# Kernel tuning notes

Measured on AMD Instinct MI355X. Metric: run time of the kernel, lower is better.

## Reference

```python
import jax, jax.numpy as jnp
import numpy as np

B, N, HID = 8, 512, 512
HEADS, HD = 16, 32
FFN, DEMB = 2048, 64
EPS = 1e-5


def layer_norm(x, g, b):
    mu = jnp.mean(x, axis=-1, keepdims=True)
    var = jnp.var(x, axis=-1, keepdims=True)
    return (x - mu) * jax.lax.rsqrt(var + EPS) * g + b


def setup_inputs() -> dict:
    key = jax.random.key(0)
    ks = jax.random.split(key, 16)
    s = lambda fan_in: 1.0 / np.sqrt(fan_in)
    return {
        "x": jax.random.normal(ks[0], (B, N, HID), jnp.float32),
        "distance_features": jax.random.normal(ks[1], (B, N, N, DEMB), jnp.float32),
        "edge_mask": jax.random.randint(ks[2], (B, N, N), 0, 2) > 0,
        "qkv_w": jax.random.uniform(ks[3], (HID, 3 * HID), jnp.float32, -s(HID), s(HID)),
        "qkv_b": jnp.zeros((3 * HID,), jnp.float32),
        "out_w": jax.random.uniform(ks[4], (HID, HID), jnp.float32, -s(HID), s(HID)),
        "out_b": jnp.zeros((HID,), jnp.float32),
        "dist_w": jax.random.uniform(ks[5], (DEMB, HEADS), jnp.float32, -s(DEMB), s(DEMB)),
        "dist_b": jnp.zeros((HEADS,), jnp.float32),
        "ln1_g": jnp.ones((HID,), jnp.float32),
        "ln1_b": jnp.zeros((HID,), jnp.float32),
        "ln2_g": jnp.ones((HID,), jnp.float32),
        "ln2_b": jnp.zeros((HID,), jnp.float32),
        "ff1_w": jax.random.uniform(ks[6], (HID, FFN), jnp.float32, -s(HID), s(HID)),
        "ff1_b": jnp.zeros((FFN,), jnp.float32),
        "ff2_w": jax.random.uniform(ks[7], (FFN, HID), jnp.float32, -s(FFN), s(FFN)),
        "ff2_b": jnp.zeros((HID,), jnp.float32),
    }


def reference(x, distance_features, edge_mask, qkv_w, qkv_b, out_w, out_b,
              dist_w, dist_b, ln1_g, ln1_b, ln2_g, ln2_b,
              ff1_w, ff1_b, ff2_w, ff2_b):
    residual = x
    h = layer_norm(x, ln1_g, ln1_b)
    qkv = h @ qkv_w + qkv_b  # [B,N,3*HID]
    q, k, v = jnp.split(qkv, 3, axis=-1)
    q = q.reshape(B, N, HEADS, HD)
    k = k.reshape(B, N, HEADS, HD)
    v = v.reshape(B, N, HEADS, HD)
    scale = jnp.sqrt(jnp.float32(HD))
    scores = jnp.einsum('bihd,bjhd->bhij', q, k) / scale  # [B,H,N,N]
    bias = distance_features @ dist_w + dist_b  # [B,N,N,H]
    scores = scores + jnp.transpose(bias, (0, 3, 1, 2))
    neg = jnp.finfo(scores.dtype).min
    scores = jnp.where(edge_mask[:, None, :, :], scores, neg)
    attn = jax.nn.softmax(scores, axis=-1)
    ctx = jnp.einsum('bhij,bjhd->bihd', attn, v).reshape(B, N, HID)
    x = residual + ctx @ out_w + out_b
    y = layer_norm(x, ln2_g, ln2_b)
    ff = jax.nn.gelu(y @ ff1_w + ff1_b, approximate=False) @ ff2_w + ff2_b
    return x + ff
```

## Files before the change

### kernel.cpp

```cpp
#include <hip/hip_runtime.h>
#include <cstddef>
#include <cstdint>

#define B_     8
#define N_     512
#define HID_   512
#define HEADS_ 16
#define HD_    32
#define FFN_   2048
#define DEMB_  64
#define ROWS   (B_*N_)

typedef unsigned short u16;
typedef short bf16x8 __attribute__((ext_vector_type(8)));
typedef float f32x4  __attribute__((ext_vector_type(4)));
typedef short short8v __attribute__((ext_vector_type(8)));
typedef short short4v __attribute__((ext_vector_type(4)));

__device__ __forceinline__ u16 f2bf(float f) {
  unsigned u = __float_as_uint(f);
  u += 0x7fffu + ((u >> 16) & 1u);
  return (u16)(u >> 16);
}
__device__ __forceinline__ float bf2f(u16 b) {
  return __uint_as_float(((unsigned)b) << 16);
}

__device__ __forceinline__ void gload16(const void* g, void* l) {
  __builtin_amdgcn_global_load_lds(
      (const __attribute__((address_space(1))) unsigned int*)g,
      (__attribute__((address_space(3))) unsigned int*)l, 16, 0, 0);
}

__global__ void detect_mask_kernel(const unsigned char* __restrict__ m,
                                   int* __restrict__ flag) {
  int t = blockIdx.x * blockDim.x + threadIdx.x;
  if ((t & 3) != 0) {
    if (m[t] != 0) atomicOr(flag, 1);
  }
}

__global__ __launch_bounds__(256) void ln_kernel(const float* __restrict__ x,
                                                 const float* __restrict__ g,
                                                 const float* __restrict__ bt,
                                                 u16* __restrict__ y) {
  const int lane = threadIdx.x & 63;
  const int row  = blockIdx.x * 4 + (threadIdx.x >> 6);
  const float* xr = x + (size_t)row * HID_;
  float4 v0 = *(const float4*)(xr + lane * 8);
  float4 v1 = *(const float4*)(xr + lane * 8 + 4);
  float s = v0.x + v0.y + v0.z + v0.w + v1.x + v1.y + v1.z + v1.w;
  float q = v0.x*v0.x + v0.y*v0.y + v0.z*v0.z + v0.w*v0.w
          + v1.x*v1.x + v1.y*v1.y + v1.z*v1.z + v1.w*v1.w;
  #pragma unroll
  for (int off = 32; off > 0; off >>= 1) {
    s += __shfl_xor(s, off, 64);
    q += __shfl_xor(q, off, 64);
  }
  const float mean = s * (1.0f / HID_);
  const float var  = q * (1.0f / HID_) - mean * mean;
  const float rs   = rsqrtf(var + 1e-5f);
  const float4 g0 = *(const float4*)(g + lane * 8);
  const float4 g1 = *(const float4*)(g + lane * 8 + 4);
  const float4 b0 = *(const float4*)(bt + lane * 8);
  const float4 b1 = *(const float4*)(bt + lane * 8 + 4);
  short8v o;
  o[0] = (short)f2bf((v0.x - mean) * rs * g0.x + b0.x);
  o[1] = (short)f2bf((v0.y - mean) * rs * g0.y + b0.y);
  o[2] = (short)f2bf((v0.z - mean) * rs * g0.z + b0.z);
  o[3] = (short)f2bf((v0.w - mean) * rs * g0.w + b0.w);
  o[4] = (short)f2bf((v1.x - mean) * rs * g1.x + b1.x);
  o[5] = (short)f2bf((v1.y - mean) * rs * g1.y + b1.y);
  o[6] = (short)f2bf((v1.z - mean) * rs * g1.z + b1.z);
  o[7] = (short)f2bf((v1.w - mean) * rs * g1.w + b1.w);
  *(short8v*)(y + (size_t)row * HID_ + lane * 8) = o;
}

__global__ __launch_bounds__(256) void wt_kernel(const float* __restrict__ W,
                                                 u16* __restrict__ Wt,
                                                 int K, int N) {
  __shared__ float tile[32][33];
  const int t = threadIdx.x;
  const int n0 = blockIdx.x * 32, k0 = blockIdx.y * 32;
  const int tx = t & 31, ty = t >> 5;
  #pragma unroll
  for (int i = 0; i < 4; ++i)
    tile[ty + 8 * i][tx] = W[(size_t)(k0 + ty + 8 * i) * N + n0 + tx];
  __syncthreads();
  #pragma unroll
  for (int i = 0; i < 4; ++i) {
    const int n = ty + 8 * i;
    Wt[(size_t)(n0 + n) * K + k0 + tx] = f2bf(tile[tx][n]);
  }
}

template <int ACT, bool HAS_RES, bool OUT_BF16>
__global__ __launch_bounds__(256) void mfma_gemm(
    const u16* __restrict__ A, const u16* __restrict__ Wt,
    const float* __restrict__ bias, const float* __restrict__ res,
    void* __restrict__ Cout, int N, int K) {
  __shared__ __align__(16) u16 As[128 * 64];
  __shared__ __align__(16) u16 Bs[128 * 64];
  const int t    = threadIdx.x;
  const int wid  = t >> 6, lane = t & 63;
  const int wr   = wid >> 1, wc = wid & 1;
  const int m0   = blockIdx.y * 128, n0 = blockIdx.x * 128;
  const int srow8 = lane >> 3;
  const int sslot = (lane & 7) ^ srow8;

  f32x4 zero = {0.f, 0.f, 0.f, 0.f};
  f32x4 acc[4][4];
  #pragma unroll
  for (int m = 0; m < 4; ++m)
    #pragma unroll
    for (int n = 0; n < 4; ++n) acc[m][n] = zero;

  for (int kt = 0; kt < K; kt += 64) {
    __syncthreads();
    #pragma unroll
    for (int i = 0; i < 4; ++i) {
      const int rbase = wid * 32 + i * 8;
      const int r = rbase + srow8;
      gload16(A  + (size_t)(m0 + r) * K + kt + sslot * 8, &As[rbase * 64]);
      gload16(Wt + (size_t)(n0 + r) * K + kt + sslot * 8, &Bs[rbase * 64]);
    }
    __syncthreads();
    #pragma unroll
    for (int kk = 0; kk < 2; ++kk) {
      bf16x8 a[4], b[4];
      #pragma unroll
      for (int m = 0; m < 4; ++m) {
        const int row = wr * 64 + m * 16 + (lane & 15);
        const int s   = (kk * 4 + (lane >> 4)) ^ (row & 7);
        a[m] = *(const bf16x8*)&As[row * 64 + s * 8];
      }
      #pragma unroll
      for (int n = 0; n < 4; ++n) {
        const int row = wc * 64 + n * 16 + (lane & 15);
        const int s   = (kk * 4 + (lane >> 4)) ^ (row & 7);
        b[n] = *(const bf16x8*)&Bs[row * 64 + s * 8];
      }
      #pragma unroll
      for (int m = 0; m < 4; ++m)
        #pragma unroll
        for (int n = 0; n < 4; ++n)
          acc[m][n] = __builtin_amdgcn_mfma_f32_16x16x32_bf16(
              a[m], b[n], acc[m][n], 0, 0, 0);
    }
  }
  #pragma unroll
  for (int n = 0; n < 4; ++n) {
    const int col = n0 + wc * 64 + n * 16 + (lane & 15);
    const float bb = bias[col];
    #pragma unroll
    for (int m = 0; m < 4; ++m) {
      #pragma unroll
      for (int j = 0; j < 4; ++j) {
        const int row = m0 + wr * 64 + m * 16 + (lane >> 4) * 4 + j;
        float v = acc[m][n][j] + bb;
        if (ACT == 1) v = 0.5f * v * (1.0f + erff(v * 0.70710678118654752f));
        const size_t off = (size_t)row * N + col;
        if (HAS_RES) v += res[off];
        if (OUT_BF16) ((u16*)Cout)[off] = f2bf(v);
        else          ((float*)Cout)[off] = v;
      }
    }
  }
}

__global__ __launch_bounds__(256) void bias_kernel(
    const float* __restrict__ df, const unsigned char* __restrict__ mask8,
    const float* __restrict__ dw, const float* __restrict__ db,
    const int* __restrict__ flag, u16* __restrict__ biasb) {
  __shared__ float dfs[128][68];
  const int t    = threadIdx.x;
  const int tile = blockIdx.x & 3;
  const int i    = (blockIdx.x >> 2) & 511;
  const int b    = blockIdx.x >> 11;
  const int j0   = tile * 128;
  const int h    = t >> 4;
  const int jt   = t & 15;

  const float4* gsrc =
      (const float4*)(df + (((size_t)b * N_ + i) * N_ + j0) * DEMB_);
  #pragma unroll
  for (int s = 0; s < 8; ++s) {
    const int f   = s * 256 + t;
    const int row = f >> 4, d4 = f & 15;
    *(float4*)&dfs[row][d4 * 4] = gsrc[f];
  }

  float4 w[16];
  #pragma unroll
  for (int d4 = 0; d4 < 16; ++d4) {
    w[d4].x = dw[(d4 * 4 + 0) * HEADS_ + h];
    w[d4].y = dw[(d4 * 4 + 1) * HEADS_ + h];
    w[d4].z = dw[(d4 * 4 + 2) * HEADS_ + h];
    w[d4].w = dw[(d4 * 4 + 3) * HEADS_ + h];
  }
  const float bh = db[h];
  const int fb = *flag;
  const int* mask32 = (const int*)mask8;
  const size_t mbase = ((size_t)b * N_ + i) * N_ + j0;
  u16* obase = biasb + (((size_t)b * HEADS_ + h) * N_ + i) * N_ + j0;
  __syncthreads();

  for (int s = 0; s < 8; ++s) {
    const int jl = s * 16 + jt;
    float a0 = 0.f, a1 = 0.f, a2 = 0.f, a3 = 0.f;
    #pragma unroll
    for (int d4 = 0; d4 < 16; ++d4) {
      const float4 v = *(const float4*)&dfs[jl][d4 * 4];
      a0 += v.x * w[d4].x;
      a1 += v.y * w[d4].y;
      a2 += v.z * w[d4].z;
      a3 += v.w * w[d4].w;
    }
    const float acc = (a0 + a1) + (a2 + a3) + bh;
    const bool mv = fb ? (mask8[mbase + jl] != 0) : (mask32[mbase + jl] != 0);
    obase[jl] = f2bf(mv ? acc : -1e30f);
  }
}

__global__ __launch_bounds__(256) void attn_kernel(
    const float* __restrict__ qkv, const u16* __restrict__ biasb,
    u16* __restrict__ ctx) {
  __shared__ union {
    u16 k[N_ * HD_];
    struct {
      float po[3][64][33];
      float pm[3][64];
      float pl[3][64];
    } c;
  } sm;
  const int t    = threadIdx.x;
  const int bx   = blockIdx.x;
  const int b    = bx >> 7;
  const int h    = (bx >> 3) & 15;
  const int iblk = bx & 7;
  const int jq   = t >> 6;
  const int r    = t & 63;
  const int i    = iblk * 64 + r;
  const size_t qbase = (size_t)b * N_ * (3 * HID_);

  for (int idx = t; idx < N_ * 8; idx += 256) {
    const int j = idx >> 3, f = idx & 7;
    const float4 kv = *(const float4*)(qkv + qbase + (size_t)j * (3 * HID_) +
                                       HID_ + h * HD_ + f * 4);
    short4v ks;
    ks[0] = (short)f2bf(kv.x); ks[1] = (short)f2bf(kv.y);
    ks[2] = (short)f2bf(kv.z); ks[3] = (short)f2bf(kv.w);
    *(short4v*)&sm.k[j * HD_ + f * 4] = ks;
  }
  __syncthreads();

  float q[HD_];
  {
    const float* qp = qkv + qbase + (size_t)i * (3 * HID_) + h * HD_;
    #pragma unroll
    for (int f = 0; f < 8; ++f) {
      const float4 v = *(const float4*)(qp + f * 4);
      q[f*4+0] = v.x * 0.17677669529663687f;
      q[f*4+1] = v.y * 0.17677669529663687f;
      q[f*4+2] = v.z * 0.17677669529663687f;
      q[f*4+3] = v.w * 0.17677669529663687f;
    }
  }
  const u16* brow = biasb + (((size_t)b * HEADS_ + h) * N_ + i) * N_ + jq * 128;
  const float* vbase = qkv + qbase + 2 * HID_ + h * HD_;
  float m = -3.0e38f, l = 0.f;
  float o[HD_];
  #pragma unroll
  for (int d = 0; d < HD_; ++d) o[d] = 0.f;

  for (int j8 = 0; j8 < 128; j8 += 8) {
    const short8v bq = *(const short8v*)(brow + j8);
    #pragma unroll
    for (int e = 0; e < 8; ++e) {
      const int j = jq * 128 + j8 + e;
      const u16* kr = &sm.k[j * HD_];
      float s = 0.f;
      #pragma unroll
      for (int c = 0; c < 4; ++c) {
        const short8v kk = *(const short8v*)(kr + c * 8);
        #pragma unroll
        for (int d = 0; d < 8; ++d)
          s += q[c*8+d] * bf2f((u16)kk[d]);
      }
      s += bf2f((u16)bq[e]);
      if (s - m > 8.0f) {
        const float corr = __expf(m - s);
        l *= corr;
        #pragma unroll
        for (int d = 0; d < HD_; ++d) o[d] *= corr;
        m = s;
      }
      const float p = __expf(s - m);
      l += p;
      const float4* vr = (const float4*)(vbase + (size_t)j * (3 * HID_));
      #pragma unroll
      for (int c = 0; c < 8; ++c) {
        const float4 vv = vr[c];
        o[c*4+0] += p * vv.x; o[c*4+1] += p * vv.y;
        o[c*4+2] += p * vv.z; o[c*4+3] += p * vv.w;
      }
    }
  }

  __syncthreads();
  if (jq > 0) {
    sm.c.pm[jq-1][r] = m;
    sm.c.pl[jq-1][r] = l;
    #pragma unroll
    for (int d = 0; d < HD_; ++d) sm.c.po[jq-1][r][d] = o[d];
  }
  __syncthreads();
  if (jq == 0) {
    #pragma unroll
    for (int p2 = 0; p2 < 3; ++p2) {
      const float m2 = sm.c.pm[p2][r], l2 = sm.c.pl[p2][r];
      const float mn = fmaxf(m, m2);
      const float c1 = __expf(m - mn), c2 = __expf(m2 - mn);
      l = l * c1 + l2 * c2;
      #pragma unroll
      for (int d = 0; d < HD_; ++d)
        o[d] = o[d] * c1 + sm.c.po[p2][r][d] * c2;
      m = mn;
    }
    const float inv = 1.0f / l;
    u16* cp = ctx + (((size_t)b * N_ + i) * HEADS_ + h) * HD_;
    #pragma unroll
    for (int f = 0; f < 4; ++f) {
      short8v v;
      #pragma unroll
      for (int e = 0; e < 8; ++e) v[e] = (short)f2bf(o[f*8+e] * inv);
      *(short8v*)(cp + f * 8) = v;
    }
  }
}

extern "C" void kernel_launch(void* const* d_in, const int* in_sizes, int n_in,
                              void* d_out, int out_size, void* d_ws, size_t ws_size,
                              hipStream_t stream) {
  const float* x      = (const float*)d_in[0];
  const float* df     = (const float*)d_in[1];
  const unsigned char* mask = (const unsigned char*)d_in[2];
  const float* qkv_w  = (const float*)d_in[3];
  const float* qkv_b  = (const float*)d_in[4];
  const float* out_w  = (const float*)d_in[5];
  const float* out_b  = (const float*)d_in[6];
  const float* dist_w = (const float*)d_in[7];
  const float* dist_b = (const float*)d_in[8];
  const float* ln1_g  = (const float*)d_in[9];
  const float* ln1_b  = (const float*)d_in[10];
  const float* ln2_g  = (const float*)d_in[11];
  const float* ln2_b  = (const float*)d_in[12];
  const float* ff1_w  = (const float*)d_in[13];
  const float* ff1_b  = (const float*)d_in[14];
  const float* ff2_w  = (const float*)d_in[15];
  const float* ff2_b  = (const float*)d_in[16];
  float* out = (float*)d_out;

  char* p = (char*)d_ws;
  auto alloc = [&](size_t bytes) {
    char* r = p;
    p += (bytes + 255) & ~(size_t)255;
    return r;
  };
  float* qkv    = (float*)alloc((size_t)ROWS * 3 * HID_ * 4);
  u16*   biasb  = (u16*)alloc((size_t)B_ * HEADS_ * N_ * N_ * 2);
  float* xa     = (float*)alloc((size_t)ROWS * HID_ * 4);
  u16*   h16    = (u16*)alloc((size_t)ROWS * HID_ * 2);
  u16*   ctx16  = (u16*)alloc((size_t)ROWS * HID_ * 2);
  u16*   y16    = (u16*)alloc((size_t)ROWS * HID_ * 2);
  u16*   ff116  = (u16*)alloc((size_t)ROWS * FFN_ * 2);
  u16*   qkv_wt = (u16*)alloc((size_t)3 * HID_ * HID_ * 2);
  u16*   out_wt = (u16*)alloc((size_t)HID_ * HID_ * 2);
  u16*   ff1_wt = (u16*)alloc((size_t)FFN_ * HID_ * 2);
  u16*   ff2_wt = (u16*)alloc((size_t)HID_ * FFN_ * 2);
  int*   flag   = (int*)alloc(sizeof(int));

  hipMemsetAsync(flag, 0, sizeof(int), stream);
  detect_mask_kernel<<<256, 256, 0, stream>>>(mask, flag);

  wt_kernel<<<dim3(3 * HID_ / 32, HID_ / 32), 256, 0, stream>>>(qkv_w, qkv_wt, HID_, 3 * HID_);
  wt_kernel<<<dim3(HID_ / 32, HID_ / 32), 256, 0, stream>>>(out_w, out_wt, HID_, HID_);
  wt_kernel<<<dim3(FFN_ / 32, HID_ / 32), 256, 0, stream>>>(ff1_w, ff1_wt, HID_, FFN_);
  wt_kernel<<<dim3(HID_ / 32, FFN_ / 32), 256, 0, stream>>>(ff2_w, ff2_wt, FFN_, HID_);

  ln_kernel<<<ROWS / 4, 256, 0, stream>>>(x, ln1_g, ln1_b, h16);
  mfma_gemm<0, false, false><<<dim3(3 * HID_ / 128, ROWS / 128), 256, 0, stream>>>(
      h16, qkv_wt, qkv_b, nullptr, qkv, 3 * HID_, HID_);
  bias_kernel<<<B_ * N_ * 4, 256, 0, stream>>>(df, mask, dist_w, dist_b, flag, biasb);
  attn_kernel<<<B_ * HEADS_ * 8, 256, 0, stream>>>(qkv, biasb, ctx16);
  mfma_gemm<0, true, false><<<dim3(HID_ / 128, ROWS / 128), 256, 0, stream>>>(
      ctx16, out_wt, out_b, x, xa, HID_, HID_);
  ln_kernel<<<ROWS / 4, 256, 0, stream>>>(xa, ln2_g, ln2_b, y16);
  mfma_gemm<1, false, true><<<dim3(FFN_ / 128, ROWS / 128), 256, 0, stream>>>(
      y16, ff1_wt, ff1_b, nullptr, ff116, FFN_, HID_);
  mfma_gemm<0, true, false><<<dim3(HID_ / 128, ROWS / 128), 256, 0, stream>>>(
      ff116, ff2_wt, ff2_b, xa, out, HID_, FFN_);
}
```

Before: 529.8 us.

## Merge weight-prep launches and stage bias outputs in LDS for vector stores

Measured after the change: 465.2 us. 1.14x faster.

```diff
diff --git a/kernel.cpp b/kernel.cpp
--- a/kernel.cpp
+++ b/kernel.cpp
@@ -32,11 +32,42 @@
       (__attribute__((address_space(3))) unsigned int*)l, 16, 0, 0);
 }
 
-__global__ void detect_mask_kernel(const unsigned char* __restrict__ m,
-                                   int* __restrict__ flag) {
-  int t = blockIdx.x * blockDim.x + threadIdx.x;
-  if ((t & 3) != 0) {
-    if (m[t] != 0) atomicOr(flag, 1);
+__device__ __forceinline__ void wt_tile(const float* __restrict__ W,
+                                        u16* __restrict__ Wt,
+                                        int K, int N, int tt, int tid) {
+  __shared__ float tile[32][33];
+  const int nt = N / 32;
+  const int n0 = (tt % nt) * 32, k0 = (tt / nt) * 32;
+  const int tx = tid & 31, ty = tid >> 5;
+  #pragma unroll
+  for (int i = 0; i < 4; ++i)
+    tile[ty + 8 * i][tx] = W[(size_t)(k0 + ty + 8 * i) * N + n0 + tx];
+  __syncthreads();
+  #pragma unroll
+  for (int i = 0; i < 4; ++i) {
+    const int n = ty + 8 * i;
+    Wt[(size_t)(n0 + n) * K + k0 + tx] = f2bf(tile[tx][n]);
+  }
+}
+
+__global__ __launch_bounds__(256) void prep_kernel(
+    const float* __restrict__ qkv_w, const float* __restrict__ out_w,
+    const float* __restrict__ ff1_w, const float* __restrict__ ff2_w,
+    u16* __restrict__ qkv_wt, u16* __restrict__ out_wt,
+    u16* __restrict__ ff1_wt, u16* __restrict__ ff2_wt,
+    const unsigned char* __restrict__ mask, int* __restrict__ flag) {
+  const int bid = blockIdx.x, t = threadIdx.x;
+  if (bid < 768) {
+    wt_tile(qkv_w, qkv_wt, HID_, 3 * HID_, bid, t);
+  } else if (bid < 1024) {
+    wt_tile(out_w, out_wt, HID_, HID_, bid - 768, t);
+  } else if (bid < 2048) {
+    wt_tile(ff1_w, ff1_wt, HID_, FFN_, bid - 1024, t);
+  } else if (bid < 3072) {
+    wt_tile(ff2_w, ff2_wt, FFN_, HID_, bid - 2048, t);
+  } else {
+    const int idx = (bid - 3072) * 256 + t;
+    if ((idx & 3) != 0 && mask[idx] != 0) atomicOr(flag, 1);
   }
 }
 
@@ -76,24 +107,6 @@
   *(short8v*)(y + (size_t)row * HID_ + lane * 8) = o;
 }
 
-__global__ __launch_bounds__(256) void wt_kernel(const float* __restrict__ W,
-                                                 u16* __restrict__ Wt,
-                                                 int K, int N) {
-  __shared__ float tile[32][33];
-  const int t = threadIdx.x;
-  const int n0 = blockIdx.x * 32, k0 = blockIdx.y * 32;
-  const int tx = t & 31, ty = t >> 5;
-  #pragma unroll
-  for (int i = 0; i < 4; ++i)
-    tile[ty + 8 * i][tx] = W[(size_t)(k0 + ty + 8 * i) * N + n0 + tx];
-  __syncthreads();
-  #pragma unroll
-  for (int i = 0; i < 4; ++i) {
-    const int n = ty + 8 * i;
-    Wt[(size_t)(n0 + n) * K + k0 + tx] = f2bf(tile[tx][n]);
-  }
-}
-
 template <int ACT, bool HAS_RES, bool OUT_BF16>
 __global__ __launch_bounds__(256) void mfma_gemm(
     const u16* __restrict__ A, const u16* __restrict__ Wt,
@@ -173,6 +186,8 @@
     const float* __restrict__ dw, const float* __restrict__ db,
     const int* __restrict__ flag, u16* __restrict__ biasb) {
   __shared__ float dfs[128][68];
+  __shared__ u16 obuf[HEADS_][128];
+  __shared__ unsigned char mbuf[128];
   const int t    = threadIdx.x;
   const int tile = blockIdx.x & 3;
   const int i    = (blockIdx.x >> 2) & 511;
@@ -186,8 +201,12 @@
   #pragma unroll
   for (int s = 0; s < 8; ++s) {
     const int f   = s * 256 + t;
-    const int row = f >> 4, d4 = f & 15;
-    *(float4*)&dfs[row][d4 * 4] = gsrc[f];
+    *(float4*)&dfs[f >> 4][(f & 15) * 4] = gsrc[f];
+  }
+  const int fb = *flag;
+  if (t < 128) {
+    const size_t midx = ((size_t)b * N_ + i) * N_ + j0 + t;
+    mbuf[t] = fb ? (mask8[midx] != 0) : (((const int*)mask8)[midx] != 0);
   }
 
   float4 w[16];
@@ -199,12 +218,9 @@
     w[d4].w = dw[(d4 * 4 + 3) * HEADS_ + h];
   }
   const float bh = db[h];
-  const int fb = *flag;
-  const int* mask32 = (const int*)mask8;
-  const size_t mbase = ((size_t)b * N_ + i) * N_ + j0;
-  u16* obase = biasb + (((size_t)b * HEADS_ + h) * N_ + i) * N_ + j0;
-  __syncthreads();
-
+  __syncthreads();
+
+  #pragma unroll
   for (int s = 0; s < 8; ++s) {
     const int jl = s * 16 + jt;
     float a0 = 0.f, a1 = 0.f, a2 = 0.f, a3 = 0.f;
@@ -217,9 +233,12 @@
       a3 += v.w * w[d4].w;
     }
     const float acc = (a0 + a1) + (a2 + a3) + bh;
-    const bool mv = fb ? (mask8[mbase + jl] != 0) : (mask32[mbase + jl] != 0);
-    obase[jl] = f2bf(mv ? acc : -1e30f);
-  }
+    obuf[h][jl] = f2bf(mbuf[jl] ? acc : -1e30f);
+  }
+  __syncthreads();
+  const int h2 = t >> 4, c = t & 15;
+  u16* ob = biasb + (((size_t)b * HEADS_ + h2) * N_ + i) * N_ + j0;
+  *(short8v*)(ob + c * 8) = *(const short8v*)&obuf[h2][c * 8];
 }
 
 __global__ __launch_bounds__(256) void attn_kernel(
@@ -381,13 +400,9 @@
   int*   flag   = (int*)alloc(sizeof(int));
 
   hipMemsetAsync(flag, 0, sizeof(int), stream);
-  detect_mask_kernel<<<256, 256, 0, stream>>>(mask, flag);
-
-  wt_kernel<<<dim3(3 * HID_ / 32, HID_ / 32), 256, 0, stream>>>(qkv_w, qkv_wt, HID_, 3 * HID_);
-  wt_kernel<<<dim3(HID_ / 32, HID_ / 32), 256, 0, stream>>>(out_w, out_wt, HID_, HID_);
-  wt_kernel<<<dim3(FFN_ / 32, HID_ / 32), 256, 0, stream>>>(ff1_w, ff1_wt, HID_, FFN_);
-  wt_kernel<<<dim3(HID_ / 32, FFN_ / 32), 256, 0, stream>>>(ff2_w, ff2_wt, FFN_, HID_);
-
+  prep_kernel<<<3328, 256, 0, stream>>>(qkv_w, out_w, ff1_w, ff2_w,
+                                        qkv_wt, out_wt, ff1_wt, ff2_wt,
+                                        mask, flag);
   ln_kernel<<<ROWS / 4, 256, 0, stream>>>(x, ln1_g, ln1_b, h16);
   mfma_gemm<0, false, false><<<dim3(3 * HID_ / 128, ROWS / 128), 256, 0, stream>>>(
       h16, qkv_wt, qkv_b, nullptr, qkv, 3 * HID_, HID_);
```
